# Optimization experiments

Hardware: AMD Instinct MI355X
Metric: run time of the kernel (lower is better)

The kernel has to match this reference:

```python
import jax, jax.numpy as jnp
import numpy as np

NUM_TYPES = 16
D_IN = 256
D_OUT = 256
N = 262144


def setup_inputs() -> dict:
    key = jax.random.key(0)
    k_x, k_idx, k_w = jax.random.split(key, 3)
    x = jax.random.normal(k_x, (N, D_IN), dtype=jnp.float32)
    idx = jax.random.randint(k_idx, (N,), 0, NUM_TYPES, dtype=jnp.int64)
    # One weight matrix per type; e3nn-style normalization 1/sqrt(d_in)
    W = jax.random.normal(k_w, (NUM_TYPES, D_IN, D_OUT), dtype=jnp.float32) / jnp.sqrt(
        jnp.float32(D_IN)
    )
    return {"x": x, "idx": idx, "W": W}


def reference(x, idx, W):
    # Per-element indexed linear: out[n] = x[n] @ W[idx[n]].
    # Avoid gathering a [N, d_in, d_out] weight tensor: mask inputs per type
    # and run one dense GEMM per type (T is a small fixed constant).
    num_types = W.shape[0]
    out = jnp.zeros((x.shape[0], W.shape[-1]), dtype=x.dtype)
    for t in range(num_types):
        mask = (idx == t).astype(x.dtype)[:, None]  # [N, 1]
        out = out + (x * mask) @ W[t]
    return out
```

## Files before the change

kernel.cpp:

```cpp
#include <hip/hip_runtime.h>
#include <hip/hip_bf16.h>


#define NTYPES 16
#define TROWS 32
#define GRID_BLOCKS 512

typedef __bf16 bf16x8 __attribute__((ext_vector_type(8)));
typedef float f32x4 __attribute__((ext_vector_type(4)));

static __device__ __forceinline__ unsigned int f2bf_pk(float a, float b) {
  unsigned int ua = __float_as_uint(a);
  unsigned int ub = __float_as_uint(b);
  ua = (ua + 0x7FFFu + ((ua >> 16) & 1u)) >> 16;
  ub = (ub + 0x7FFFu + ((ub >> 16) & 1u)) >> 16;
  return ua | (ub << 16);
}

static __device__ __forceinline__ unsigned int cvtpk(float a, float b) {
  unsigned int r;
  asm("v_cvt_pk_bf16_f32 %0, %1, %2" : "=v"(r) : "v"(a), "v"(b));
  return r;
}

static __device__ __forceinline__ void load16_lds(const float* g, float* l) {
  __builtin_amdgcn_global_load_lds(
      (const __attribute__((address_space(1))) unsigned int*)g,
      (__attribute__((address_space(3))) unsigned int*)l, 16, 0, 0);
}


__global__ void zero_meta_kernel(unsigned int* meta) {
  if (threadIdx.x < 128) meta[threadIdx.x] = 0;
}

__global__ void hist_kernel(const int* __restrict__ idx, int N,
                            unsigned int* __restrict__ meta) {
  __shared__ unsigned int h[NTYPES];
  if (threadIdx.x < NTYPES) h[threadIdx.x] = 0;
  __syncthreads();
  for (int n = blockIdx.x * 256 + threadIdx.x; n < N; n += gridDim.x * 256)
    atomicAdd(&h[idx[n] & 15], 1u);
  __syncthreads();
  if (threadIdx.x < NTYPES) atomicAdd(&meta[threadIdx.x], h[threadIdx.x]);
}

__global__ void prefix_kernel(unsigned int* meta) {
  if (threadIdx.x == 0) {
    unsigned int o = 0, ts = 0;
    for (int t = 0; t < NTYPES; t++) {
      meta[16 + t] = o;
      meta[32 + t] = o;
      meta[48 + t] = ts;
      o += meta[t];
      ts += (meta[t] + (TROWS - 1)) / TROWS;
    }
    meta[64] = ts;
  }
}

__global__ void tiles_kernel(const unsigned int* __restrict__ meta,
                             uint2* __restrict__ desc, int maxTiles) {
  __shared__ unsigned int ts[17], offs[16], cnts[16];
  if (threadIdx.x < 17) ts[threadIdx.x] = meta[48 + threadIdx.x];
  if (threadIdx.x < 16) {
    offs[threadIdx.x] = meta[16 + threadIdx.x];
    cnts[threadIdx.x] = meta[threadIdx.x];
  }
  __syncthreads();
  int tile = blockIdx.x * 256 + threadIdx.x;
  if (tile >= maxTiles) return;
  uint2 d = make_uint2(0u, 0u);
  if ((unsigned)tile < ts[16]) {
    int t = 0;
    while ((unsigned)tile >= ts[t + 1]) t++;
    unsigned int rowbase = offs[t] + ((unsigned)tile - ts[t]) * TROWS;
    unsigned int rem = offs[t] + cnts[t] - rowbase;
    unsigned int nrows = rem < (unsigned)TROWS ? rem : (unsigned)TROWS;
    d = make_uint2(rowbase, (unsigned)t | (nrows << 8));
  }
  desc[tile] = d;
}

__global__ void scatter_kernel(const int* __restrict__ idx, int N,
                               unsigned int* __restrict__ meta,
                               int* __restrict__ perm) {
  __shared__ unsigned int h[NTYPES];
  __shared__ unsigned int base[NTYPES];
  int b0 = blockIdx.x * 4096;
  if (threadIdx.x < NTYPES) h[threadIdx.x] = 0;
  __syncthreads();
  unsigned int lr[16];
  int tt[16];
#pragma unroll
  for (int i = 0; i < 16; i++) {
    int n = b0 + i * 256 + threadIdx.x;
    int t = (n < N) ? (idx[n] & 15) : 0;
    tt[i] = t;
    lr[i] = (n < N) ? atomicAdd(&h[t], 1u) : 0u;
  }
  __syncthreads();
  if (threadIdx.x < NTYPES)
    base[threadIdx.x] = atomicAdd(&meta[32 + threadIdx.x], h[threadIdx.x]);
  __syncthreads();
#pragma unroll
  for (int i = 0; i < 16; i++) {
    int n = b0 + i * 256 + threadIdx.x;
    if (n < N) perm[base[tt[i]] + lr[i]] = n;
  }
}

__global__ void packW_kernel(const float* __restrict__ W,
                             unsigned short* __restrict__ Wp) {
  int id = blockIdx.x * 256 + threadIdx.x;
  int c = id & 255;
  int tk = id >> 8;
  const float* src = W + (size_t)tk * 32 * 256 + c;
  unsigned int buf[16];
#pragma unroll
  for (int p = 0; p < 16; p++)
    buf[p] = f2bf_pk(src[(2 * p) * 256], src[(2 * p + 1) * 256]);
  uint4* d4 = (uint4*)(Wp + (size_t)id * 32);
#pragma unroll
  for (int p = 0; p < 4; p++)
    d4[p] = make_uint4(buf[4 * p], buf[4 * p + 1], buf[4 * p + 2], buf[4 * p + 3]);
}

__global__ __launch_bounds__(256, 2) void gemm_kernel(
    const float* __restrict__ x, const unsigned short* __restrict__ Wp,
    const int* __restrict__ perm, const uint2* __restrict__ desc,
    float* __restrict__ out, float* __restrict__ dump, int maxTiles) {
  __shared__ float ldsx[2][TROWS * 256];
  __shared__ int permS[2][TROWS];

  int tpb = maxTiles / GRID_BLOCKS;
  int rem = maxTiles - tpb * GRID_BLOCKS;
  int b = blockIdx.x;
  int base = b * tpb + (b < rem ? b : rem);
  int cnt = tpb + (b < rem ? 1 : 0);
  if (cnt <= 0) return;

  int tid = threadIdx.x;
  int l = tid & 63, w = tid >> 6;
  int lm = l & 15, lh = l >> 4;
  int clampT = maxTiles - 1;
  int myrow = w * 8 + (l & 7);

  uint2 dscC = desc[base];
  uint2 dscN = desc[base + 1 <= clampT ? base + 1 : clampT];
  uint2 dscN2 = desc[base + 2 <= clampT ? base + 2 : clampT];

  int prCur, prNxt;
  {
    int nr = (int)(dscC.y >> 8);
    prCur = (myrow < nr) ? perm[dscC.x + myrow] : 0;
  }
  {
    int nr = (int)(dscN.y >> 8);
    prNxt = (cnt > 1 && myrow < nr) ? perm[dscN.x + myrow] : 0;
  }

  if (l < 8) permS[0][w * 8 + l] = prCur;
#pragma unroll
  for (int j = 0; j < 8; ++j) {
    int prj = __shfl(prCur, j);
    const float* src = x + (size_t)prj * 256 + ((l ^ j) << 2);
    load16_lds(src, &ldsx[0][(w * 8 + j) * 256]);
  }
  __syncthreads();

  int buf = 0;
  int tCached = -1;
  bf16x8 wfr[32];
  const uint4* Wp4 = (const uint4*)Wp;
  float* dumpP = dump + (size_t)tid * 16;

  for (int it = 0; it < cnt; ++it) {
    int nrowsC = (int)(dscC.y >> 8);
    int tC = (int)(dscC.y & 15u);

    if (it + 1 < cnt) {
      if (l < 8) permS[buf ^ 1][w * 8 + l] = prNxt;
#pragma unroll
      for (int j = 0; j < 8; ++j) {
        int prj = __shfl(prNxt, j);
        const float* src = x + (size_t)prj * 256 + ((l ^ j) << 2);
        load16_lds(src, &ldsx[buf ^ 1][(w * 8 + j) * 256]);
      }
    }
    int prN2 = 0;
    if (it + 2 < cnt) {
      int nr2 = (int)(dscN2.y >> 8);
      if (myrow < nr2) prN2 = perm[dscN2.x + myrow];
    }
    int i3 = base + it + 3;
    uint2 dscN3 = desc[i3 <= clampT ? i3 : clampT];

    if (tC != tCached) {
      tCached = tC;
      const uint4* Wt = Wp4 + (size_t)tC * 8 * 256 * 4;
#pragma unroll
      for (int kk = 0; kk < 8; kk++)
#pragma unroll
        for (int fn = 0; fn < 4; fn++)
          wfr[kk * 4 + fn] = __builtin_bit_cast(
              bf16x8, Wt[(size_t)(kk * 256 + w * 64 + fn * 16 + lm) * 4 + lh]);
    }

    f32x4 acc[2][4];
#pragma unroll
    for (int i = 0; i < 2; i++)
#pragma unroll
      for (int j = 0; j < 4; j++) acc[i][j] = (f32x4){0.f, 0.f, 0.f, 0.f};

#pragma unroll
    for (int kk = 0; kk < 8; kk++) {
      bf16x8 a[2];
#pragma unroll
      for (int fm = 0; fm < 2; fm++) {
        int r2 = fm * 16 + lm;
        const float4* rowp = (const float4*)&ldsx[buf][r2 * 256];
        int c0 = kk * 8 + lh * 2;
        int s = r2 & 7;
        float4 f0 = rowp[c0 ^ s];
        float4 f1 = rowp[(c0 + 1) ^ s];
        uint4 v;
        v.x = cvtpk(f0.x, f0.y);
        v.y = cvtpk(f0.z, f0.w);
        v.z = cvtpk(f1.x, f1.y);
        v.w = cvtpk(f1.z, f1.w);
        a[fm] = __builtin_bit_cast(bf16x8, v);
      }
#pragma unroll
      for (int fn = 0; fn < 4; fn++) {
        acc[0][fn] = __builtin_amdgcn_mfma_f32_16x16x32_bf16(
            a[0], wfr[kk * 4 + fn], acc[0][fn], 0, 0, 0);
        acc[1][fn] = __builtin_amdgcn_mfma_f32_16x16x32_bf16(
            a[1], wfr[kk * 4 + fn], acc[1][fn], 0, 0, 0);
      }
    }

#pragma unroll
    for (int fm = 0; fm < 2; fm++) {
#pragma unroll
      for (int r_ = 0; r_ < 4; r_++) {
        int rit = fm * 16 + lh * 4 + r_;
        bool valid = rit < nrowsC;
        int grow = permS[buf][rit & (TROWS - 1)];
        float* orow = out + (size_t)grow * 256 + w * 64 + lm;
#pragma unroll
        for (int fn = 0; fn < 4; fn++)
          __builtin_nontemporal_store(acc[fm][fn][r_],
                                      valid ? orow + fn * 16 : dumpP + fn);
      }
    }

    asm volatile("s_waitcnt vmcnt(32) lgkmcnt(0)\n\ts_barrier" ::: "memory");

    buf ^= 1;
    dscC = dscN;
    dscN = dscN2;
    dscN2 = dscN3;
    prCur = prNxt;
    prNxt = prN2;
  }
}

extern "C" void kernel_launch(void* const* d_in, const int* in_sizes, int n_in,
                              void* d_out, int out_size, void* d_ws,
                              size_t ws_size, hipStream_t stream) {
  const float* x = (const float*)d_in[0];
  const int* idx = (const int*)d_in[1];
  const float* W = (const float*)d_in[2];
  float* out = (float*)d_out;
  int N = in_sizes[0] / 256;
  int maxTiles = N / TROWS + NTYPES;

  unsigned int* meta = (unsigned int*)d_ws;
  float* dump = (float*)((char*)d_ws + 512);
  uint2* desc = (uint2*)((char*)d_ws + 512 + 65536);
  int* perm = (int*)((char*)d_ws + 512 + 65536 + (size_t)maxTiles * 8);
  unsigned short* Wp =
      (unsigned short*)((char*)d_ws + 512 + 65536 + (size_t)maxTiles * 8 +
                        (size_t)N * 4);

  zero_meta_kernel<<<1, 128, 0, stream>>>(meta);
  hist_kernel<<<256, 256, 0, stream>>>(idx, N, meta);
  prefix_kernel<<<1, 64, 0, stream>>>(meta);
  packW_kernel<<<128, 256, 0, stream>>>(W, Wp);
  tiles_kernel<<<(maxTiles + 255) / 256, 256, 0, stream>>>(meta, desc,
                                                           maxTiles);
  int nScatter = (N + 4095) / 4096;
  scatter_kernel<<<nScatter, 256, 0, stream>>>(idx, N, meta, perm);

  gemm_kernel<<<GRID_BLOCKS, 256, 0, stream>>>(x, Wp, perm, desc, out, dump,
                                               maxTiles);
}
```

Baseline: 163.7 us.

## Halve GEMM tile rows, triple-buffer x loads, and split columns over 8 waves

The GEMM kernel now works on 16-row tiles with a 3-deep LDS ring buffer, so row gathers are prefetched two tiles ahead instead of one. Blocks grow to 512 threads (8 waves), and each wave owns 32 output columns, which halves its per-wave weight-fragment registers and accumulators. Descriptor and permutation prefetching are deepened to match, the waitcnt threshold is retuned, and output stores become regular rather than nontemporal. The intent is to hide gather latency in this memory-bound kernel and raise occupancy. In exchange there are twice as many tiles with smaller MFMA work per barrier, and the extra barriers may add overhead.

```diff
diff --git a/kernel.cpp b/kernel.cpp
--- a/kernel.cpp
+++ b/kernel.cpp
@@ -3,7 +3,8 @@
 
 
 #define NTYPES 16
-#define TROWS 32
+#define TROWS 16
+#define NBUF 3
 #define GRID_BLOCKS 512
 
 typedef __bf16 bf16x8 __attribute__((ext_vector_type(8)));
@@ -126,12 +127,12 @@
     d4[p] = make_uint4(buf[4 * p], buf[4 * p + 1], buf[4 * p + 2], buf[4 * p + 3]);
 }
 
-__global__ __launch_bounds__(256, 2) void gemm_kernel(
+__global__ __launch_bounds__(512, 2) void gemm_kernel(
     const float* __restrict__ x, const unsigned short* __restrict__ Wp,
     const int* __restrict__ perm, const uint2* __restrict__ desc,
     float* __restrict__ out, float* __restrict__ dump, int maxTiles) {
-  __shared__ float ldsx[2][TROWS * 256];
-  __shared__ int permS[2][TROWS];
+  __shared__ float ldsx[NBUF][TROWS * 256];
+  __shared__ int permS[NBUF][TROWS];
 
   int tpb = maxTiles / GRID_BLOCKS;
   int rem = maxTiles - tpb * GRID_BLOCKS;
@@ -144,57 +145,70 @@
   int l = tid & 63, w = tid >> 6;
   int lm = l & 15, lh = l >> 4;
   int clampT = maxTiles - 1;
-  int myrow = w * 8 + (l & 7);
-
-  uint2 dscC = desc[base];
-  uint2 dscN = desc[base + 1 <= clampT ? base + 1 : clampT];
-  uint2 dscN2 = desc[base + 2 <= clampT ? base + 2 : clampT];
-
-  int prCur, prNxt;
+  int myrow = 2 * w + (l & 1);
+
+  uint2 d0, d1, d2, d3;
   {
-    int nr = (int)(dscC.y >> 8);
-    prCur = (myrow < nr) ? perm[dscC.x + myrow] : 0;
-  }
-  {
-    int nr = (int)(dscN.y >> 8);
-    prNxt = (cnt > 1 && myrow < nr) ? perm[dscN.x + myrow] : 0;
-  }
-
-  if (l < 8) permS[0][w * 8 + l] = prCur;
-#pragma unroll
-  for (int j = 0; j < 8; ++j) {
-    int prj = __shfl(prCur, j);
-    const float* src = x + (size_t)prj * 256 + ((l ^ j) << 2);
-    load16_lds(src, &ldsx[0][(w * 8 + j) * 256]);
-  }
-  __syncthreads();
-
-  int buf = 0;
+    int j;
+    j = base + 0; d0 = desc[j <= clampT ? j : clampT];
+    j = base + 1; d1 = desc[j <= clampT ? j : clampT];
+    j = base + 2; d2 = desc[j <= clampT ? j : clampT];
+    j = base + 3; d3 = desc[j <= clampT ? j : clampT];
+  }
+
+  int pr0 = 0, pr1 = 0, pr2 = 0;
+  { int nr = (int)(d0.y >> 8); if (myrow < nr) pr0 = perm[d0.x + myrow]; }
+  if (cnt > 1) { int nr = (int)(d1.y >> 8); if (myrow < nr) pr1 = perm[d1.x + myrow]; }
+  if (cnt > 2) { int nr = (int)(d2.y >> 8); if (myrow < nr) pr2 = perm[d2.x + myrow]; }
+
+  if (l < 2) permS[0][myrow] = pr0;
+#pragma unroll
+  for (int j = 0; j < 2; ++j) {
+    int prj = __shfl(pr0, j);
+    int row = 2 * w + j;
+    load16_lds(x + (size_t)prj * 256 + ((l ^ (row & 7)) << 2),
+               &ldsx[0][row * 256]);
+  }
+  if (cnt > 1) {
+    if (l < 2) permS[1][myrow] = pr1;
+#pragma unroll
+    for (int j = 0; j < 2; ++j) {
+      int prj = __shfl(pr1, j);
+      int row = 2 * w + j;
+      load16_lds(x + (size_t)prj * 256 + ((l ^ (row & 7)) << 2),
+                 &ldsx[1][row * 256]);
+    }
+  }
+  __syncthreads();
+
+  int bc = 0;
   int tCached = -1;
-  bf16x8 wfr[32];
+  bf16x8 wfr[16];
   const uint4* Wp4 = (const uint4*)Wp;
   float* dumpP = dump + (size_t)tid * 16;
 
   for (int it = 0; it < cnt; ++it) {
-    int nrowsC = (int)(dscC.y >> 8);
-    int tC = (int)(dscC.y & 15u);
-
-    if (it + 1 < cnt) {
-      if (l < 8) permS[buf ^ 1][w * 8 + l] = prNxt;
-#pragma unroll
-      for (int j = 0; j < 8; ++j) {
-        int prj = __shfl(prNxt, j);
-        const float* src = x + (size_t)prj * 256 + ((l ^ j) << 2);
-        load16_lds(src, &ldsx[buf ^ 1][(w * 8 + j) * 256]);
+    int nrowsC = (int)(d0.y >> 8);
+    int tC = (int)(d0.y & 15u);
+    int bs = bc + 2; if (bs >= NBUF) bs -= NBUF;
+
+    if (it + 2 < cnt) {
+      if (l < 2) permS[bs][myrow] = pr2;
+#pragma unroll
+      for (int j = 0; j < 2; ++j) {
+        int prj = __shfl(pr2, j);
+        int row = 2 * w + j;
+        load16_lds(x + (size_t)prj * 256 + ((l ^ (row & 7)) << 2),
+                   &ldsx[bs][row * 256]);
       }
     }
-    int prN2 = 0;
-    if (it + 2 < cnt) {
-      int nr2 = (int)(dscN2.y >> 8);
-      if (myrow < nr2) prN2 = perm[dscN2.x + myrow];
-    }
-    int i3 = base + it + 3;
-    uint2 dscN3 = desc[i3 <= clampT ? i3 : clampT];
+    int pr3 = 0;
+    if (it + 3 < cnt) {
+      int nr = (int)(d3.y >> 8);
+      if (myrow < nr) pr3 = perm[d3.x + myrow];
+    }
+    uint2 d4;
+    { int j4 = base + it + 4; d4 = desc[j4 <= clampT ? j4 : clampT]; }
 
     if (tC != tCached) {
       tCached = tC;
@@ -202,67 +216,54 @@
 #pragma unroll
       for (int kk = 0; kk < 8; kk++)
 #pragma unroll
-        for (int fn = 0; fn < 4; fn++)
-          wfr[kk * 4 + fn] = __builtin_bit_cast(
-              bf16x8, Wt[(size_t)(kk * 256 + w * 64 + fn * 16 + lm) * 4 + lh]);
-    }
-
-    f32x4 acc[2][4];
-#pragma unroll
-    for (int i = 0; i < 2; i++)
-#pragma unroll
-      for (int j = 0; j < 4; j++) acc[i][j] = (f32x4){0.f, 0.f, 0.f, 0.f};
+        for (int fn = 0; fn < 2; fn++)
+          wfr[kk * 2 + fn] = __builtin_bit_cast(
+              bf16x8,
+              Wt[(size_t)(kk * 256 + w * 32 + fn * 16 + lm) * 4 + lh]);
+    }
+
+    f32x4 acc[2];
+    acc[0] = (f32x4){0.f, 0.f, 0.f, 0.f};
+    acc[1] = (f32x4){0.f, 0.f, 0.f, 0.f};
 
 #pragma unroll
     for (int kk = 0; kk < 8; kk++) {
-      bf16x8 a[2];
-#pragma unroll
-      for (int fm = 0; fm < 2; fm++) {
-        int r2 = fm * 16 + lm;
-        const float4* rowp = (const float4*)&ldsx[buf][r2 * 256];
-        int c0 = kk * 8 + lh * 2;
-        int s = r2 & 7;
-        float4 f0 = rowp[c0 ^ s];
-        float4 f1 = rowp[(c0 + 1) ^ s];
-        uint4 v;
-        v.x = cvtpk(f0.x, f0.y);
-        v.y = cvtpk(f0.z, f0.w);
-        v.z = cvtpk(f1.x, f1.y);
-        v.w = cvtpk(f1.z, f1.w);
-        a[fm] = __builtin_bit_cast(bf16x8, v);
+      const float4* rowp = (const float4*)&ldsx[bc][lm * 256];
+      int c0 = kk * 8 + lh * 2;
+      int s = lm & 7;
+      float4 f0 = rowp[c0 ^ s];
+      float4 f1 = rowp[(c0 + 1) ^ s];
+      uint4 v;
+      v.x = cvtpk(f0.x, f0.y);
+      v.y = cvtpk(f0.z, f0.w);
+      v.z = cvtpk(f1.x, f1.y);
+      v.w = cvtpk(f1.z, f1.w);
+      bf16x8 a = __builtin_bit_cast(bf16x8, v);
+      acc[0] = __builtin_amdgcn_mfma_f32_16x16x32_bf16(a, wfr[kk * 2 + 0],
+                                                       acc[0], 0, 0, 0);
+      acc[1] = __builtin_amdgcn_mfma_f32_16x16x32_bf16(a, wfr[kk * 2 + 1],
+                                                       acc[1], 0, 0, 0);
+    }
+
+#pragma unroll
+    for (int r_ = 0; r_ < 4; r_++) {
+      int rit = lh * 4 + r_;
+      bool valid = rit < nrowsC;
+      int grow = permS[bc][rit];
+      float* orow = out + (size_t)grow * 256 + w * 32 + lm;
+#pragma unroll
+      for (int fn = 0; fn < 2; fn++) {
+        float* p = valid ? orow + fn * 16 : dumpP + fn;
+        *p = acc[fn][r_];
       }
-#pragma unroll
-      for (int fn = 0; fn < 4; fn++) {
-        acc[0][fn] = __builtin_amdgcn_mfma_f32_16x16x32_bf16(
-            a[0], wfr[kk * 4 + fn], acc[0][fn], 0, 0, 0);
-        acc[1][fn] = __builtin_amdgcn_mfma_f32_16x16x32_bf16(
-            a[1], wfr[kk * 4 + fn], acc[1][fn], 0, 0, 0);
-      }
-    }
-
-#pragma unroll
-    for (int fm = 0; fm < 2; fm++) {
-#pragma unroll
-      for (int r_ = 0; r_ < 4; r_++) {
-        int rit = fm * 16 + lh * 4 + r_;
-        bool valid = rit < nrowsC;
-        int grow = permS[buf][rit & (TROWS - 1)];
-        float* orow = out + (size_t)grow * 256 + w * 64 + lm;
-#pragma unroll
-        for (int fn = 0; fn < 4; fn++)
-          __builtin_nontemporal_store(acc[fm][fn][r_],
-                                      valid ? orow + fn * 16 : dumpP + fn);
-      }
-    }
-
-    asm volatile("s_waitcnt vmcnt(32) lgkmcnt(0)\n\ts_barrier" ::: "memory");
-
-    buf ^= 1;
-    dscC = dscN;
-    dscN = dscN2;
-    dscN2 = dscN3;
-    prCur = prNxt;
-    prNxt = prN2;
+    }
+
+    asm volatile("s_waitcnt vmcnt(12) lgkmcnt(0)\n\ts_barrier" ::: "memory");
+    __builtin_amdgcn_sched_barrier(0);
+
+    bc = bc + 1 == NBUF ? 0 : bc + 1;
+    d0 = d1; d1 = d2; d2 = d3; d3 = d4;
+    pr2 = pr3;
   }
 }
 
@@ -293,6 +294,6 @@
   int nScatter = (N + 4095) / 4096;
   scatter_kernel<<<nScatter, 256, 0, stream>>>(idx, N, meta, perm);
 
-  gemm_kernel<<<GRID_BLOCKS, 256, 0, stream>>>(x, Wp, perm, desc, out, dump,
+  gemm_kernel<<<GRID_BLOCKS, 512, 0, stream>>>(x, Wp, perm, desc, out, dump,
                                                maxTiles);
 }
```

Measured after the change: 168.6 us. 3.0% more time.
